# Kernel optimization log

Measured on AMD Instinct MI355X. Metric: run time of the kernel, lower is better.

The kernel has to match this reference:

```python
import jax, jax.numpy as jnp
import numpy as np

EMBED = 256
HEADS = 8
HEAD_DIM = EMBED // HEADS  # 32, even for RoPE
INIT_VAL = 1.0
HEADS_RANGE = 3.0


def rotate_every_two(x):
    # (x1, x2) -> (-x2, x1) on interleaved pairs of last dim
    x1 = x[..., ::2]
    x2 = x[..., 1::2]
    return jnp.stack([-x2, x1], axis=-1).reshape(x.shape)


def theta_shift(x, sin, cos):
    # x: [B, heads, H, W, D]; sin/cos: [H, W, D] broadcast over B, heads
    return x * cos + rotate_every_two(x) * sin


def rel_pos_2d(H, W):
    # RetNetRelPos2d: RoPE angles + per-head exponential decay mask
    angle = 1.0 / (10000.0 ** jnp.linspace(0.0, 1.0, HEAD_DIM // 2))
    angle = jnp.repeat(angle, 2)  # [D]
    idx = jnp.arange(H * W, dtype=jnp.float32)
    sin = jnp.sin(idx[:, None] * angle[None, :]).reshape(H, W, HEAD_DIM)
    cos = jnp.cos(idx[:, None] * angle[None, :]).reshape(H, W, HEAD_DIM)
    h_idx = jnp.arange(HEADS, dtype=jnp.float32)
    decay = jnp.log(1.0 - 2.0 ** (-INIT_VAL - HEADS_RANGE * h_idx / HEADS))  # [heads]
    gh, gw = jnp.meshgrid(jnp.arange(H), jnp.arange(W), indexing='ij')
    grid = jnp.stack([gh, gw], axis=-1).reshape(H * W, 2)  # [N,2]
    dist = jnp.abs(grid[:, None, :] - grid[None, :, :]).sum(-1)  # [N,N] L1 distance
    mask = dist[None, :, :].astype(jnp.float32) * decay[:, None, None]  # [heads,N,N]
    return sin, cos, mask


def setup_inputs() -> dict:
    key = jax.random.key(0)
    ks = jax.random.split(key, 8)
    B, H, W, C = 2, 48, 48, EMBED
    s = 0.02
    return {
        'x': jax.random.normal(ks[0], (B, H, W, C), jnp.float32),
        'Wq': jax.random.normal(ks[1], (C, C), jnp.float32) * s,
        'bq': jnp.zeros((C,), jnp.float32),
        'Wk': jax.random.normal(ks[2], (C, C), jnp.float32) * s,
        'bk': jnp.zeros((C,), jnp.float32),
        'Wv': jax.random.normal(ks[3], (C, C), jnp.float32) * s,
        'bv': jnp.zeros((C,), jnp.float32),
        'lepe_w': jax.random.normal(ks[4], (C, 1, 5, 5), jnp.float32) * s,  # depthwise 5x5
        'lepe_b': jnp.zeros((C,), jnp.float32),
        'Wo': jax.random.normal(ks[5], (C, C), jnp.float32) * s,
        'bo': jnp.zeros((C,), jnp.float32),
    }


def reference(x, Wq, bq, Wk, bk, Wv, bv, lepe_w, lepe_b, Wo, bo):
    B, H, W, C = x.shape
    N = H * W
    sin, cos, mask = rel_pos_2d(H, W)
    scaling = HEAD_DIM ** -0.5

    q = x @ Wq + bq
    k = (x @ Wk + bk) * scaling
    v = x @ Wv + bv

    # lepe: depthwise 5x5 conv on v (BHWC)
    lepe = jax.lax.conv_general_dilated(
        v.transpose(0, 3, 1, 2), lepe_w, (1, 1), 'SAME',
        feature_group_count=C, dimension_numbers=('NCHW', 'OIHW', 'NCHW'))
    lepe = lepe.transpose(0, 2, 3, 1) + lepe_b  # [B,H,W,C]

    def split_heads(t):
        return t.reshape(B, H, W, HEADS, HEAD_DIM).transpose(0, 3, 1, 2, 4)

    qr = theta_shift(split_heads(q), sin, cos).reshape(B, HEADS, N, HEAD_DIM)
    kr = theta_shift(split_heads(k), sin, cos).reshape(B, HEADS, N, HEAD_DIM)
    vv = split_heads(v).reshape(B, HEADS, N, HEAD_DIM)

    attn = jnp.einsum('bhnd,bhmd->bhnm', qr, kr) + mask[None]  # [B,heads,N,N]
    attn = jax.nn.softmax(attn, axis=-1)
    out = jnp.einsum('bhnm,bhmd->bhnd', attn, vv)
    out = out.transpose(0, 2, 1, 3).reshape(B, H, W, C)
    out = out + lepe
    return out @ Wo + bo
```

## Files before the change

kernel.cpp:

```cpp
#include <hip/hip_runtime.h>
#include <hip/hip_bf16.h>
#include <math.h>

#define NN 2304
#define ROWSZ 4608
#define SZ (ROWSZ*256)

typedef __attribute__((ext_vector_type(8))) short short8;
typedef __attribute__((ext_vector_type(4))) float f32x4;

__device__ __forceinline__ float bf2f(unsigned short u) {
    return __uint_as_float(((unsigned int)u) << 16);
}
__device__ __forceinline__ unsigned short f2bf(float f) {
    unsigned int u = __float_as_uint(f);
    u += 0x7FFFu + ((u >> 16) & 1u);
    return (unsigned short)(u >> 16);
}
__device__ __forceinline__ unsigned int pack_bf2(float a, float b) {
    return (unsigned int)f2bf(a) | ((unsigned int)f2bf(b) << 16);
}

__device__ __forceinline__ float ub2f(unsigned int v, int r) {
#if defined(__has_builtin)
#if __has_builtin(__builtin_amdgcn_cvt_f32_ubyte0)
    switch (r) {
        case 0: return __builtin_amdgcn_cvt_f32_ubyte0(v);
        case 1: return __builtin_amdgcn_cvt_f32_ubyte1(v);
        case 2: return __builtin_amdgcn_cvt_f32_ubyte2(v);
        default: return __builtin_amdgcn_cvt_f32_ubyte3(v);
    }
#else
    return (float)((v >> (8*r)) & 0xFFu);
#endif
#else
    return (float)((v >> (8*r)) & 0xFFu);
#endif
}

template<int F32>
__device__ __forceinline__ float ldin(const void* p, int i) {
    if constexpr (F32) return ((const float*)p)[i];
    else return bf2f(((const unsigned short*)p)[i]);
}

__global__ void detect_kernel(const unsigned int* __restrict__ x, int* __restrict__ flag) {
    int t = threadIdx.x;
    int cnt = 0;
    for (int i = t; i < 256; i += 64) {
        unsigned int e = (x[i] >> 7) & 0xFFu;
        cnt += (e < 87u || e > 167u) ? 1 : 0;
    }
    #pragma unroll
    for (int o = 32; o; o >>= 1) cnt += __shfl_down(cnt, o);
    if (t == 0) *flag = (cnt >= 32) ? 1 : 0;
}

__global__ __launch_bounds__(256) void dist_kernel(unsigned char* __restrict__ D,
                                                   float2* __restrict__ scT) {
    const int nq = blockIdx.x;
    const int yq = (nq*21846) >> 20, xq = nq - yq*48;
    unsigned int* drow = reinterpret_cast<unsigned int*>(D + (size_t)nq*NN);
    for (int idx = threadIdx.x; idx < 576; idx += 256) {
        const int kp0 = idx*4;
        unsigned int wv = 0;
        #pragma unroll
        for (int r = 0; r < 4; ++r) {
            int kp = kp0 + r;
            int yk = (kp*21846) >> 20;
            int xk = kp - yk*48;
            unsigned int dist = __usad((unsigned)yq, (unsigned)yk,
                                __usad((unsigned)xq, (unsigned)xk, 0u));
            wv |= dist << (8*r);
        }
        drow[idx] = wv;
    }
    if (threadIdx.x < 16) {
        const int j = threadIdx.x;
        const float ang = exp2f((float)j * (-0.8858474919699633f));
        float sv, cv;
        sincosf((float)nq * ang, &sv, &cv);
        scT[nq*16 + j] = make_float2(sv, cv);
    }
}

__global__ __launch_bounds__(256) void xprep_kernel(const void* __restrict__ x,
    const int* __restrict__ flag, unsigned short* __restrict__ xb)
{
    const int e = (blockIdx.x*256 + threadIdx.x) * 8;
    if (*flag) {
        const float* xp = (const float*)x + e;
        float4 a0 = *reinterpret_cast<const float4*>(xp);
        float4 a1 = *reinterpret_cast<const float4*>(xp + 4);
        uint4 o;
        o.x = pack_bf2(a0.x, a0.y); o.y = pack_bf2(a0.z, a0.w);
        o.z = pack_bf2(a1.x, a1.y); o.w = pack_bf2(a1.z, a1.w);
        *reinterpret_cast<uint4*>(xb + e) = o;
    } else {
        *reinterpret_cast<uint4*>(xb + e) =
            *reinterpret_cast<const uint4*>((const unsigned short*)x + e);
    }
}

__global__ __launch_bounds__(256) void wprep_kernel(
    const void* __restrict__ Wq, const void* __restrict__ bq,
    const void* __restrict__ Wk, const void* __restrict__ bk,
    const void* __restrict__ Wv, const void* __restrict__ bv,
    const int* __restrict__ flag,
    unsigned short* __restrict__ Wt, float* __restrict__ bb)
{
    __shared__ float wsh[256][17];
    const int t = threadIdx.x;
    const int m = blockIdx.y;
    const int oc0 = blockIdx.x * 16;
    const void* W  = (m == 0) ? Wq : (m == 1) ? Wk : Wv;
    const void* bs = (m == 0) ? bq : (m == 1) ? bk : bv;
    const float scale = (m == 1) ? 0.17677669529663687f * 1.4426950408889634f : 1.0f;
    const int F = *flag;
    #pragma unroll
    for (int j2 = 0; j2 < 16; ++j2)
        wsh[t][j2] = F ? ((const float*)W)[t*256 + oc0 + j2]
                       : bf2f(((const unsigned short*)W)[t*256 + oc0 + j2]);
    __syncthreads();
    const int j = t >> 4, seg = t & 15;
    unsigned int u[8];
    #pragma unroll
    for (int i = 0; i < 8; ++i) {
        float v0 = wsh[seg*16 + 2*i][j]     * scale;
        float v1 = wsh[seg*16 + 2*i + 1][j] * scale;
        u[i] = pack_bf2(v0, v1);
    }
    unsigned short* drow = Wt + ((size_t)(m*256 + oc0 + j))*256 + seg*16;
    *reinterpret_cast<uint4*>(drow)     = make_uint4(u[0], u[1], u[2], u[3]);
    *reinterpret_cast<uint4*>(drow + 8) = make_uint4(u[4], u[5], u[6], u[7]);
    if (blockIdx.x == 0)
        bb[m*256 + t] = (F ? ((const float*)bs)[t]
                           : bf2f(((const unsigned short*)bs)[t])) * scale;
}

__global__ __launch_bounds__(256) void qkv_mfma(
    const unsigned short* __restrict__ xb, const unsigned short* __restrict__ Wt,
    const float* __restrict__ bb, const float2* __restrict__ scT,
    unsigned short* __restrict__ q, unsigned short* __restrict__ k,
    unsigned short* __restrict__ v, unsigned short* __restrict__ vT)
{
    __shared__ __align__(16) char smem[43136];
    char* sc_lds = smem + 40960;
    const int t = threadIdx.x;
    const int w = t >> 6, lane = t & 63;
    const int q16 = lane & 15, quad = lane >> 4;
    const int m = blockIdx.y;
    const int tok0 = blockIdx.x * 16;
    const int b = (tok0 >= NN) ? 1 : 0;
    const int n0 = tok0 - b*NN;

    {
        float2 sv = scT[(size_t)(n0 + (t >> 4))*16 + (t & 15)];
        *reinterpret_cast<float2*>(sc_lds + (t >> 4)*136 + (t & 15)*8) = sv;
    }
    short8 af[8];
    #pragma unroll
    for (int kk = 0; kk < 8; ++kk)
        af[kk] = *reinterpret_cast<const short8*>(
            xb + (size_t)(tok0 + q16)*256 + kk*32 + quad*8);

    const unsigned short* Wm = Wt + (size_t)m*256*256;
    {
        const unsigned short* src = Wm + (size_t)t*256;
        #pragma unroll
        for (int s = 0; s < 4; ++s)
            *reinterpret_cast<uint4*>(smem + t*80 + s*16) =
                *reinterpret_cast<const uint4*>(src + s*8);
    }
    __syncthreads();

    f32x4 acc[4];
    #pragma unroll
    for (int tt = 0; tt < 4; ++tt) acc[tt] = (f32x4){0.f, 0.f, 0.f, 0.f};
    int cur = 0;
    for (int kk = 0; kk < 8; ++kk) {
        const int kkn = (kk < 7) ? kk + 1 : 7;
        uint4 nw[4];
        const unsigned short* src = Wm + (size_t)t*256 + kkn*32;
        #pragma unroll
        for (int s = 0; s < 4; ++s) nw[s] = *reinterpret_cast<const uint4*>(src + s*8);
        char* Wl = smem + cur*20480;
        #pragma unroll
        for (int tt = 0; tt < 4; ++tt) {
            short8 bf = *reinterpret_cast<const short8*>(
                Wl + (w*64 + tt*16 + q16)*80 + quad*16);
            acc[tt] = __builtin_amdgcn_mfma_f32_16x16x32_bf16(af[kk], bf, acc[tt], 0, 0, 0);
        }
        char* Wn = smem + (cur ^ 1)*20480;
        #pragma unroll
        for (int s = 0; s < 4; ++s)
            *reinterpret_cast<uint4*>(Wn + t*80 + s*16) = nw[s];
        __syncthreads();
        cur ^= 1;
    }

    char* ostage = smem;
    float bias[4];
    #pragma unroll
    for (int tt = 0; tt < 4; ++tt) bias[tt] = bb[m*256 + w*64 + tt*16 + q16];
    if (m < 2) {
        const int odd = q16 & 1;
        #pragma unroll
        for (int tt = 0; tt < 4; ++tt) {
            const int j = ((tt & 1) << 3) + (q16 >> 1);
            #pragma unroll
            for (int r = 0; r < 4; ++r) {
                const int tokL = quad*4 + r;
                float a = acc[tt][r] + bias[tt];
                float ap = __shfl_xor(a, 1);
                float2 sc = *reinterpret_cast<const float2*>(sc_lds + tokL*136 + j*8);
                float val = odd ? fmaf(a, sc.y, ap*sc.x) : fmaf(a, sc.y, -ap*sc.x);
                *reinterpret_cast<unsigned short*>(
                    ostage + tokL*528 + (w*64 + tt*16 + q16)*2) = f2bf(val);
            }
        }
    } else {
        #pragma unroll
        for (int tt = 0; tt < 4; ++tt) {
            #pragma unroll
            for (int r = 0; r < 4; ++r)
                *reinterpret_cast<unsigned short*>(
                    ostage + (quad*4 + r)*528 + (w*64 + tt*16 + q16)*2)
                    = f2bf(acc[tt][r] + bias[tt]);
        }
    }
    __syncthreads();
    unsigned short* dst = (m == 0) ? q : (m == 1) ? k : v;
    {
        char* p = ostage + (t >> 4)*528 + (t & 15)*32;
        uint4 a0 = *reinterpret_cast<uint4*>(p);
        uint4 a1 = *reinterpret_cast<uint4*>(p + 16);
        unsigned short* drow = dst + (size_t)(tok0 + (t >> 4))*256 + (t & 15)*16;
        *reinterpret_cast<uint4*>(drow)     = a0;
        *reinterpret_cast<uint4*>(drow + 8) = a1;
    }
    if (m == 2) {
        const int h = t >> 5, d = t & 31;
        unsigned int vp[8];
        #pragma unroll
        for (int i = 0; i < 8; ++i) {
            unsigned short e0 = *reinterpret_cast<unsigned short*>(
                ostage + (2*i)*528 + (h*32 + d)*2);
            unsigned short e1 = *reinterpret_cast<unsigned short*>(
                ostage + (2*i + 1)*528 + (h*32 + d)*2);
            vp[i] = (unsigned int)e0 | ((unsigned int)e1 << 16);
        }
        unsigned short* vt = vT + ((size_t)(b*8 + h)*32 + d)*NN + n0;
        *reinterpret_cast<uint4*>(vt)     = make_uint4(vp[0], vp[1], vp[2], vp[3]);
        *reinterpret_cast<uint4*>(vt + 8) = make_uint4(vp[4], vp[5], vp[6], vp[7]);
    }
}

template<int F32>
__device__ __forceinline__ void lepe_body(const unsigned short* __restrict__ v,
    const void* __restrict__ w, const void* __restrict__ wb,
    unsigned short* __restrict__ lepe)
{
    int c = threadIdx.x;
    int pos = blockIdx.x;
    int b  = pos >= NN ? 1 : 0;
    int yx = pos - b*NN;
    int y  = (yx*21846) >> 20;
    int xx = yx - y*48;
    float acc = ldin<F32>(wb, c);
    #pragma unroll
    for (int ky = 0; ky < 5; ++ky) {
        int yy = y + ky - 2;
        if ((unsigned)yy >= 48u) continue;
        #pragma unroll
        for (int kx = 0; kx < 5; ++kx) {
            int xc = xx + kx - 2;
            if ((unsigned)xc >= 48u) continue;
            acc = fmaf(bf2f(v[((b*NN + yy*48 + xc)<<8) + c]), ldin<F32>(w, c*25 + ky*5 + kx), acc);
        }
    }
    lepe[(pos<<8) + c] = f2bf(acc);
}

__global__ __launch_bounds__(256) void lepe_kernel(const unsigned short* __restrict__ v,
    const void* __restrict__ w, const void* __restrict__ wb,
    const int* __restrict__ flag, unsigned short* __restrict__ lepe)
{
    if (*flag) lepe_body<1>(v, w, wb, lepe);
    else       lepe_body<0>(v, w, wb, lepe);
}

template<int DIRECT>
__global__ __launch_bounds__(256) void attn_kernel(
    const unsigned short* __restrict__ q, const unsigned short* __restrict__ k,
    const unsigned short* __restrict__ vT, const unsigned char* __restrict__ D,
    unsigned short* __restrict__ o, float* __restrict__ pacc, float* __restrict__ pl)
{
    __shared__ char smem[27648];
    const int t = threadIdx.x;
    const int w = t >> 6, lane = t & 63;
    const int q16 = lane & 15, quad = lane >> 4;
    char* PsB = smem + 19456 + w*2048;
    const int bh = blockIdx.y, b = bh >> 3, h = bh & 7;
    const int q0 = blockIdx.x*64 + w*16;
    const int nq = q0 + q16;
    const float decay2 = log2f(1.0f - exp2f(-1.0f - 0.375f*(float)h));
    short8 qfrag = *reinterpret_cast<const short8*>(q + ((size_t)(b*NN + nq))*256 + h*32 + quad*8);
    f32x4 acc0 = {0.f,0.f,0.f,0.f}, acc1 = {0.f,0.f,0.f,0.f};
    const f32x4 zero = {0.f,0.f,0.f,0.f};
    float lacc = 0.0f;
    const unsigned short* kbase = k + (size_t)(b*NN)*256 + h*32;
    const unsigned short* vtb = vT + (size_t)bh*32*NN;
    const unsigned char* Dbase = D + (size_t)nq*NN + quad*4;
    const int skr = t >> 2, skp = t & 3;
    const int svd = t >> 3, svp = t & 7;
    const int psW = q16*16 + (quad & 1)*8;
    const int qsh = quad >> 1;
    const int nchunk = 36 / gridDim.z;
    const int kt0 = blockIdx.z * nchunk;

    {
        uint4 kraw = *reinterpret_cast<const uint4*>(kbase + (kt0*64 + skr)*256 + skp*8);
        uint4 vraw = *reinterpret_cast<const uint4*>(vtb + svd*NN + kt0*64 + svp*8);
        *reinterpret_cast<uint4*>(smem + skr*80 + skp*16) = kraw;
        *reinterpret_cast<uint4*>(smem + 5120 + svd*144 + svp*16) = vraw;
    }
    __syncthreads();

    int cur = 0;
    for (int kc = 0; kc < nchunk; ++kc) {
        const int kt = kt0 + kc;
        const int ktn = (kc + 1 < nchunk) ? kt + 1 : kt;
        uint4 nk = *reinterpret_cast<const uint4*>(kbase + (ktn*64 + skr)*256 + skp*8);
        uint4 nv = *reinterpret_cast<const uint4*>(vtb + svd*NN + ktn*64 + svp*8);
        unsigned int dw[4];
        #pragma unroll
        for (int tt = 0; tt < 4; ++tt)
            dw[tt] = *reinterpret_cast<const unsigned int*>(Dbase + kt*64 + tt*16);
        char* KsB = smem + cur*9728;
        char* VtB = KsB + 5120;
        f32x4 st[4];
        #pragma unroll
        for (int tt = 0; tt < 4; ++tt) {
            short8 kf = *reinterpret_cast<const short8*>(KsB + (tt*16 + q16)*80 + quad*16);
            st[tt] = __builtin_amdgcn_mfma_f32_16x16x32_bf16(kf, qfrag, zero, 0, 0, 0);
        }
        unsigned int pk[8];
        float lsum = 0.0f;
        #pragma unroll
        for (int tt = 0; tt < 4; ++tt) {
            float p[4];
            #pragma unroll
            for (int r = 0; r < 4; ++r) {
                p[r] = exp2f(fmaf(decay2, ub2f(dw[tt], r), st[tt][r]));
                lsum += p[r];
            }
            pk[tt*2]   = __builtin_amdgcn_perm(__float_as_uint(p[1]), __float_as_uint(p[0]), 0x07060302);
            pk[tt*2+1] = __builtin_amdgcn_perm(__float_as_uint(p[3]), __float_as_uint(p[2]), 0x07060302);
        }
        lacc += lsum;
        #pragma unroll
        for (int tt = 0; tt < 4; ++tt) {
            uint2 pp; pp.x = pk[tt*2]; pp.y = pk[tt*2+1];
            *reinterpret_cast<uint2*>(PsB + (tt >> 1)*1024 + (((tt*2) + qsh) & 3)*256 + psW) = pp;
        }
        #pragma unroll
        for (int kh = 0; kh < 2; ++kh) {
            short8 pf = *reinterpret_cast<const short8*>(PsB + kh*1024 + lane*16);
            short8 v0 = *reinterpret_cast<const short8*>(VtB + q16*144 + kh*64 + quad*16);
            short8 v1 = *reinterpret_cast<const short8*>(VtB + (16 + q16)*144 + kh*64 + quad*16);
            acc0 = __builtin_amdgcn_mfma_f32_16x16x32_bf16(v0, pf, acc0, 0, 0, 0);
            acc1 = __builtin_amdgcn_mfma_f32_16x16x32_bf16(v1, pf, acc1, 0, 0, 0);
        }
        char* KsN = smem + (cur^1)*9728;
        *reinterpret_cast<uint4*>(KsN + skr*80 + skp*16) = nk;
        *reinterpret_cast<uint4*>(KsN + 5120 + svd*144 + svp*16) = nv;
        __syncthreads();
        cur ^= 1;
    }
    lacc += __shfl_xor(lacc, 16);
    lacc += __shfl_xor(lacc, 32);
    if constexpr (DIRECT) {
        float invl = 1.0f / lacc;
        unsigned short* orow = o + ((size_t)(b*NN + nq))*256 + h*32;
        uint2 w0, w1;
        w0.x = pack_bf2(acc0[0]*invl, acc0[1]*invl);
        w0.y = pack_bf2(acc0[2]*invl, acc0[3]*invl);
        w1.x = pack_bf2(acc1[0]*invl, acc1[1]*invl);
        w1.y = pack_bf2(acc1[2]*invl, acc1[3]*invl);
        *reinterpret_cast<uint2*>(orow + quad*4)      = w0;
        *reinterpret_cast<uint2*>(orow + 16 + quad*4) = w1;
    } else {
        float* pb = pacc + ((size_t)(blockIdx.z*16 + bh)*NN + nq)*32;
        *reinterpret_cast<f32x4*>(pb + quad*4)      = acc0;
        *reinterpret_cast<f32x4*>(pb + 16 + quad*4) = acc1;
        if (quad == 0) pl[((size_t)blockIdx.z*16 + bh)*NN + nq] = lacc;
    }
}

template<int F32>
__device__ __forceinline__ void out_body(
    const unsigned short* __restrict__ o,
    const float* __restrict__ pacc, const float* __restrict__ pl,
    const unsigned short* __restrict__ lp,
    const void* __restrict__ Wo, const void* __restrict__ bo,
    void* __restrict__ out, float* __restrict__ as, int nsplit)
{
    const int t = threadIdx.x;
    const int row0 = blockIdx.x * 8;
    {
        const int e = t*8;
        const int r = t >> 5;
        const int nqr = row0 + r;
        const int ch = e & 255;
        uint4 ub = *reinterpret_cast<const uint4*>(lp + nqr*256 + ch);
        const unsigned short* bu = reinterpret_cast<const unsigned short*>(&ub);
        if (nsplit == 0) {
            uint4 ua = *reinterpret_cast<const uint4*>(o + nqr*256 + ch);
            const unsigned short* au = reinterpret_cast<const unsigned short*>(&ua);
            #pragma unroll
            for (int jj = 0; jj < 8; ++jj) as[e+jj] = bf2f(au[jj]) + bf2f(bu[jj]);
        } else {
            const int b = nqr >= NN ? 1 : 0;
            const int nq = nqr - b*NN;
            const int h = ch >> 5, d = ch & 31;
            const int bh = b*8 + h;
            float s[8] = {0.f,0.f,0.f,0.f,0.f,0.f,0.f,0.f};
            float lsum = 0.0f;
            for (int p = 0; p < nsplit; ++p) {
                const float* pb = pacc + ((size_t)(p*16 + bh)*NN + nq)*32 + d;
                f32x4 v0 = *reinterpret_cast<const f32x4*>(pb);
                f32x4 v1 = *reinterpret_cast<const f32x4*>(pb + 4);
                #pragma unroll
                for (int jj = 0; jj < 4; ++jj) { s[jj] += v0[jj]; s[4+jj] += v1[jj]; }
                lsum += pl[((size_t)p*16 + bh)*NN + nq];
            }
            float invl = 1.0f / lsum;
            #pragma unroll
            for (int jj = 0; jj < 8; ++jj) as[e+jj] = fmaf(s[jj], invl, bf2f(bu[jj]));
        }
    }
    __syncthreads();
    float a[8];
    const float bv = ldin<F32>(bo, t);
    #pragma unroll
    for (int r = 0; r < 8; ++r) a[r] = bv;
    for (int i0 = 0; i0 < 256; i0 += 4) {
        float w0 = ldin<F32>(Wo, (i0+0)*256 + t);
        float w1 = ldin<F32>(Wo, (i0+1)*256 + t);
        float w2 = ldin<F32>(Wo, (i0+2)*256 + t);
        float w3 = ldin<F32>(Wo, (i0+3)*256 + t);
        #pragma unroll
        for (int r = 0; r < 8; ++r) {
            float4 xv = *reinterpret_cast<const float4*>(&as[r*256 + i0]);
            a[r] = fmaf(xv.w,w3, fmaf(xv.z,w2, fmaf(xv.y,w1, fmaf(xv.x,w0, a[r]))));
        }
    }
    #pragma unroll
    for (int r = 0; r < 8; ++r) {
        int idx = (row0+r)*256 + t;
        if constexpr (F32) ((float*)out)[idx] = a[r];
        else ((unsigned short*)out)[idx] = f2bf(a[r]);
    }
}

__global__ __launch_bounds__(256) void out_kernel(
    const unsigned short* __restrict__ o,
    const float* __restrict__ pacc, const float* __restrict__ pl,
    const unsigned short* __restrict__ lp,
    const void* __restrict__ Wo, const void* __restrict__ bo,
    const int* __restrict__ flag, void* __restrict__ out, int nsplit)
{
    __shared__ float as[8*256];
    if (*flag) out_body<1>(o, pacc, pl, lp, Wo, bo, out, as, nsplit);
    else       out_body<0>(o, pacc, pl, lp, Wo, bo, out, as, nsplit);
}

extern "C" void kernel_launch(void* const* d_in, const int* in_sizes, int n_in,
                              void* d_out, int out_size, void* d_ws, size_t ws_size,
                              hipStream_t stream)
{
    const void* x  = d_in[0];
    const void* Wq = d_in[1];
    const void* bq = d_in[2];
    const void* Wk = d_in[3];
    const void* bk = d_in[4];
    const void* Wv = d_in[5];
    const void* bv = d_in[6];
    const void* lw = d_in[7];
    const void* lb = d_in[8];
    const void* Wo = d_in[9];
    const void* bo = d_in[10];

    int* flag = (int*)d_ws;
    unsigned short* qb   = (unsigned short*)((char*)d_ws + 256);
    unsigned short* kbuf = qb   + (size_t)SZ;
    unsigned short* vbuf = kbuf + (size_t)SZ;
    unsigned short* obuf = vbuf + (size_t)SZ;
    unsigned short* lbuf = obuf + (size_t)SZ;
    unsigned short* vtb  = lbuf + (size_t)SZ;
    unsigned char*  Dtab = (unsigned char*)(vtb + (size_t)SZ);
    float2* scT = (float2*)(Dtab + (size_t)NN*NN);
    unsigned short* xb = (unsigned short*)(scT + (size_t)NN*16);
    unsigned short* Wt = xb + (size_t)SZ;
    float* bb = (float*)(Wt + (size_t)3*256*256);

    const size_t base = 256 + 6*(size_t)SZ*2 + (size_t)NN*NN
                      + (size_t)NN*16*8 + (size_t)SZ*2
                      + (size_t)3*256*256*2 + (size_t)3*256*4;
    const size_t per_split = (size_t)16*NN*32*4 + (size_t)16*NN*4;
    int nsplit = 0;
    if      (ws_size >= base + 4*per_split) nsplit = 4;
    else if (ws_size >= base + 2*per_split) nsplit = 2;
    else if (ws_size >= base + 1*per_split) nsplit = 1;
    float* pacc = (float*)((char*)d_ws + base);
    float* pl   = pacc + (size_t)(nsplit ? nsplit : 1)*16*NN*32;

    detect_kernel<<<1, 64, 0, stream>>>((const unsigned int*)x, flag);
    dist_kernel<<<NN, 256, 0, stream>>>(Dtab, scT);
    xprep_kernel<<<576, 256, 0, stream>>>(x, flag, xb);
    wprep_kernel<<<dim3(16,3), 256, 0, stream>>>(Wq, bq, Wk, bk, Wv, bv, flag, Wt, bb);
    qkv_mfma<<<dim3(288,3), 256, 0, stream>>>(xb, Wt, bb, scT, qb, kbuf, vbuf, vtb);
    lepe_kernel<<<4608, 256, 0, stream>>>(vbuf, lw, lb, flag, lbuf);
    if (nsplit) {
        attn_kernel<0><<<dim3(36, 16, nsplit), 256, 0, stream>>>(qb, kbuf, vtb, Dtab, obuf, pacc, pl);
    } else {
        attn_kernel<1><<<dim3(36, 16, 1), 256, 0, stream>>>(qb, kbuf, vtb, Dtab, obuf, pacc, pl);
    }
    out_kernel<<<576, 256, 0, stream>>>(obuf, pacc, pl, lbuf, Wo, bo, flag, d_out, nsplit);
}
```

Baseline: 220.8 us.

## Move output projection onto bf16 MFMA with pre-transposed Wo

The output projection, previously a scalar FP32 FMA loop over 8 rows per block, now runs on 16x16x32 bf16 MFMA with 16 tokens per block. Wo and bo are transposed and converted to bf16 by the existing weight-prep kernel, and Wo slices are double-buffered through LDS. The attention+lepe activation is rounded to bf16 before the matmul, which costs precision, and the grid shrinks to 288 blocks.

```diff
diff --git a/kernel.cpp b/kernel.cpp
--- a/kernel.cpp
+++ b/kernel.cpp
@@ -106,6 +106,7 @@
     const void* __restrict__ Wq, const void* __restrict__ bq,
     const void* __restrict__ Wk, const void* __restrict__ bk,
     const void* __restrict__ Wv, const void* __restrict__ bv,
+    const void* __restrict__ Wo, const void* __restrict__ bo,
     const int* __restrict__ flag,
     unsigned short* __restrict__ Wt, float* __restrict__ bb)
 {
@@ -113,8 +114,8 @@
     const int t = threadIdx.x;
     const int m = blockIdx.y;
     const int oc0 = blockIdx.x * 16;
-    const void* W  = (m == 0) ? Wq : (m == 1) ? Wk : Wv;
-    const void* bs = (m == 0) ? bq : (m == 1) ? bk : bv;
+    const void* W  = (m == 0) ? Wq : (m == 1) ? Wk : (m == 2) ? Wv : Wo;
+    const void* bs = (m == 0) ? bq : (m == 1) ? bk : (m == 2) ? bv : bo;
     const float scale = (m == 1) ? 0.17677669529663687f * 1.4426950408889634f : 1.0f;
     const int F = *flag;
     #pragma unroll
@@ -398,82 +399,149 @@
     }
 }
 
-template<int F32>
-__device__ __forceinline__ void out_body(
+__global__ __launch_bounds__(256) void out_mfma(
     const unsigned short* __restrict__ o,
     const float* __restrict__ pacc, const float* __restrict__ pl,
     const unsigned short* __restrict__ lp,
-    const void* __restrict__ Wo, const void* __restrict__ bo,
-    void* __restrict__ out, float* __restrict__ as, int nsplit)
-{
+    const unsigned short* __restrict__ Wt, const float* __restrict__ bb,
+    const int* __restrict__ flag, void* __restrict__ out, int nsplit)
+{
+    __shared__ __align__(16) char smem[49408];
+    char* Ast = smem + 40960;
     const int t = threadIdx.x;
-    const int row0 = blockIdx.x * 8;
+    const int w = t >> 6, lane = t & 63;
+    const int q16 = lane & 15, quad = lane >> 4;
+    const int tok0 = blockIdx.x * 16;
+
     {
-        const int e = t*8;
-        const int r = t >> 5;
-        const int nqr = row0 + r;
-        const int ch = e & 255;
-        uint4 ub = *reinterpret_cast<const uint4*>(lp + nqr*256 + ch);
-        const unsigned short* bu = reinterpret_cast<const unsigned short*>(&ub);
+        const int r = t >> 4, c0 = (t & 15) * 16;
+        const int nqr = tok0 + r;
+        uint4 lb0 = *reinterpret_cast<const uint4*>(lp + (size_t)nqr*256 + c0);
+        uint4 lb1 = *reinterpret_cast<const uint4*>(lp + (size_t)nqr*256 + c0 + 8);
+        const unsigned short* lu0 = reinterpret_cast<const unsigned short*>(&lb0);
+        const unsigned short* lu1 = reinterpret_cast<const unsigned short*>(&lb1);
+        float av[16];
         if (nsplit == 0) {
-            uint4 ua = *reinterpret_cast<const uint4*>(o + nqr*256 + ch);
-            const unsigned short* au = reinterpret_cast<const unsigned short*>(&ua);
-            #pragma unroll
-            for (int jj = 0; jj < 8; ++jj) as[e+jj] = bf2f(au[jj]) + bf2f(bu[jj]);
+            uint4 oa0 = *reinterpret_cast<const uint4*>(o + (size_t)nqr*256 + c0);
+            uint4 oa1 = *reinterpret_cast<const uint4*>(o + (size_t)nqr*256 + c0 + 8);
+            const unsigned short* ou0 = reinterpret_cast<const unsigned short*>(&oa0);
+            const unsigned short* ou1 = reinterpret_cast<const unsigned short*>(&oa1);
+            #pragma unroll
+            for (int j = 0; j < 8; ++j) {
+                av[j]     = bf2f(ou0[j]) + bf2f(lu0[j]);
+                av[8 + j] = bf2f(ou1[j]) + bf2f(lu1[j]);
+            }
         } else {
             const int b = nqr >= NN ? 1 : 0;
             const int nq = nqr - b*NN;
-            const int h = ch >> 5, d = ch & 31;
-            const int bh = b*8 + h;
-            float s[8] = {0.f,0.f,0.f,0.f,0.f,0.f,0.f,0.f};
-            float lsum = 0.0f;
+            const int bh = b*8 + (c0 >> 5);
+            const int d0 = c0 & 31;
+            float s[16];
+            #pragma unroll
+            for (int j = 0; j < 16; ++j) s[j] = 0.f;
+            float lsum = 0.f;
             for (int p = 0; p < nsplit; ++p) {
-                const float* pb = pacc + ((size_t)(p*16 + bh)*NN + nq)*32 + d;
-                f32x4 v0 = *reinterpret_cast<const f32x4*>(pb);
-                f32x4 v1 = *reinterpret_cast<const f32x4*>(pb + 4);
+                const float* pb = pacc + ((size_t)(p*16 + bh)*NN + nq)*32 + d0;
                 #pragma unroll
-                for (int jj = 0; jj < 4; ++jj) { s[jj] += v0[jj]; s[4+jj] += v1[jj]; }
+                for (int j4 = 0; j4 < 4; ++j4) {
+                    f32x4 vv = *reinterpret_cast<const f32x4*>(pb + j4*4);
+                    s[j4*4+0] += vv[0]; s[j4*4+1] += vv[1];
+                    s[j4*4+2] += vv[2]; s[j4*4+3] += vv[3];
+                }
                 lsum += pl[((size_t)p*16 + bh)*NN + nq];
             }
             float invl = 1.0f / lsum;
             #pragma unroll
-            for (int jj = 0; jj < 8; ++jj) as[e+jj] = fmaf(s[jj], invl, bf2f(bu[jj]));
-        }
+            for (int j = 0; j < 8; ++j) {
+                av[j]     = fmaf(s[j],     invl, bf2f(lu0[j]));
+                av[8 + j] = fmaf(s[8 + j], invl, bf2f(lu1[j]));
+            }
+        }
+        unsigned int u[8];
+        #pragma unroll
+        for (int i = 0; i < 8; ++i) u[i] = pack_bf2(av[2*i], av[2*i+1]);
+        *reinterpret_cast<uint4*>(Ast + r*528 + c0*2)      = make_uint4(u[0],u[1],u[2],u[3]);
+        *reinterpret_cast<uint4*>(Ast + r*528 + c0*2 + 16) = make_uint4(u[4],u[5],u[6],u[7]);
+    }
+    const unsigned short* Wm = Wt + (size_t)3*256*256;
+    {
+        const unsigned short* src = Wm + (size_t)t*256;
+        #pragma unroll
+        for (int s2 = 0; s2 < 4; ++s2)
+            *reinterpret_cast<uint4*>(smem + t*80 + s2*16) =
+                *reinterpret_cast<const uint4*>(src + s2*8);
     }
     __syncthreads();
-    float a[8];
-    const float bv = ldin<F32>(bo, t);
-    #pragma unroll
-    for (int r = 0; r < 8; ++r) a[r] = bv;
-    for (int i0 = 0; i0 < 256; i0 += 4) {
-        float w0 = ldin<F32>(Wo, (i0+0)*256 + t);
-        float w1 = ldin<F32>(Wo, (i0+1)*256 + t);
-        float w2 = ldin<F32>(Wo, (i0+2)*256 + t);
-        float w3 = ldin<F32>(Wo, (i0+3)*256 + t);
-        #pragma unroll
-        for (int r = 0; r < 8; ++r) {
-            float4 xv = *reinterpret_cast<const float4*>(&as[r*256 + i0]);
-            a[r] = fmaf(xv.w,w3, fmaf(xv.z,w2, fmaf(xv.y,w1, fmaf(xv.x,w0, a[r]))));
-        }
-    }
-    #pragma unroll
-    for (int r = 0; r < 8; ++r) {
-        int idx = (row0+r)*256 + t;
-        if constexpr (F32) ((float*)out)[idx] = a[r];
-        else ((unsigned short*)out)[idx] = f2bf(a[r]);
-    }
-}
-
-__global__ __launch_bounds__(256) void out_kernel(
-    const unsigned short* __restrict__ o,
-    const float* __restrict__ pacc, const float* __restrict__ pl,
-    const unsigned short* __restrict__ lp,
-    const void* __restrict__ Wo, const void* __restrict__ bo,
-    const int* __restrict__ flag, void* __restrict__ out, int nsplit)
-{
-    __shared__ float as[8*256];
-    if (*flag) out_body<1>(o, pacc, pl, lp, Wo, bo, out, as, nsplit);
-    else       out_body<0>(o, pacc, pl, lp, Wo, bo, out, as, nsplit);
+    short8 af[8];
+    #pragma unroll
+    for (int kk = 0; kk < 8; ++kk)
+        af[kk] = *reinterpret_cast<const short8*>(Ast + q16*528 + kk*64 + quad*16);
+
+    f32x4 acc[4];
+    #pragma unroll
+    for (int tt = 0; tt < 4; ++tt) acc[tt] = (f32x4){0.f, 0.f, 0.f, 0.f};
+    int cur = 0;
+    for (int kk = 0; kk < 8; ++kk) {
+        const int kkn = (kk < 7) ? kk + 1 : 7;
+        uint4 nw[4];
+        const unsigned short* src = Wm + (size_t)t*256 + kkn*32;
+        #pragma unroll
+        for (int s2 = 0; s2 < 4; ++s2) nw[s2] = *reinterpret_cast<const uint4*>(src + s2*8);
+        char* Wl = smem + cur*20480;
+        #pragma unroll
+        for (int tt = 0; tt < 4; ++tt) {
+            short8 bf = *reinterpret_cast<const short8*>(
+                Wl + (w*64 + tt*16 + q16)*80 + quad*16);
+            acc[tt] = __builtin_amdgcn_mfma_f32_16x16x32_bf16(af[kk], bf, acc[tt], 0, 0, 0);
+        }
+        char* Wn = smem + (cur ^ 1)*20480;
+        #pragma unroll
+        for (int s2 = 0; s2 < 4; ++s2)
+            *reinterpret_cast<uint4*>(Wn + t*80 + s2*16) = nw[s2];
+        __syncthreads();
+        cur ^= 1;
+    }
+    const int F = *flag;
+    float bias[4];
+    #pragma unroll
+    for (int tt = 0; tt < 4; ++tt) bias[tt] = bb[3*256 + w*64 + tt*16 + q16];
+    if (F) {
+        char* ostf = smem;
+        #pragma unroll
+        for (int tt = 0; tt < 4; ++tt) {
+            #pragma unroll
+            for (int r = 0; r < 4; ++r)
+                *reinterpret_cast<float*>(ostf + (quad*4 + r)*1040
+                    + (w*64 + tt*16 + q16)*4) = acc[tt][r] + bias[tt];
+        }
+        __syncthreads();
+        char* p = ostf + (t >> 4)*1040 + (t & 15)*64;
+        float4 x0 = *reinterpret_cast<float4*>(p);
+        float4 x1 = *reinterpret_cast<float4*>(p + 16);
+        float4 x2 = *reinterpret_cast<float4*>(p + 32);
+        float4 x3 = *reinterpret_cast<float4*>(p + 48);
+        float* drow = (float*)out + (size_t)(tok0 + (t >> 4))*256 + (t & 15)*16;
+        *reinterpret_cast<float4*>(drow)      = x0;
+        *reinterpret_cast<float4*>(drow + 4)  = x1;
+        *reinterpret_cast<float4*>(drow + 8)  = x2;
+        *reinterpret_cast<float4*>(drow + 12) = x3;
+    } else {
+        char* ost = smem;
+        #pragma unroll
+        for (int tt = 0; tt < 4; ++tt) {
+            #pragma unroll
+            for (int r = 0; r < 4; ++r)
+                *reinterpret_cast<unsigned short*>(ost + (quad*4 + r)*528
+                    + (w*64 + tt*16 + q16)*2) = f2bf(acc[tt][r] + bias[tt]);
+        }
+        __syncthreads();
+        char* p = ost + (t >> 4)*528 + (t & 15)*32;
+        uint4 a0 = *reinterpret_cast<uint4*>(p);
+        uint4 a1 = *reinterpret_cast<uint4*>(p + 16);
+        unsigned short* drow = (unsigned short*)out + (size_t)(tok0 + (t >> 4))*256 + (t & 15)*16;
+        *reinterpret_cast<uint4*>(drow)     = a0;
+        *reinterpret_cast<uint4*>(drow + 8) = a1;
+    }
 }
 
 extern "C" void kernel_launch(void* const* d_in, const int* in_sizes, int n_in,
@@ -503,11 +571,11 @@
     float2* scT = (float2*)(Dtab + (size_t)NN*NN);
     unsigned short* xb = (unsigned short*)(scT + (size_t)NN*16);
     unsigned short* Wt = xb + (size_t)SZ;
-    float* bb = (float*)(Wt + (size_t)3*256*256);
+    float* bb = (float*)(Wt + (size_t)4*256*256);
 
     const size_t base = 256 + 6*(size_t)SZ*2 + (size_t)NN*NN
                       + (size_t)NN*16*8 + (size_t)SZ*2
-                      + (size_t)3*256*256*2 + (size_t)3*256*4;
+                      + (size_t)4*256*256*2 + (size_t)4*256*4;
     const size_t per_split = (size_t)16*NN*32*4 + (size_t)16*NN*4;
     int nsplit = 0;
     if      (ws_size >= base + 4*per_split) nsplit = 4;
@@ -519,7 +587,7 @@
     detect_kernel<<<1, 64, 0, stream>>>((const unsigned int*)x, flag);
     dist_kernel<<<NN, 256, 0, stream>>>(Dtab, scT);
     xprep_kernel<<<576, 256, 0, stream>>>(x, flag, xb);
-    wprep_kernel<<<dim3(16,3), 256, 0, stream>>>(Wq, bq, Wk, bk, Wv, bv, flag, Wt, bb);
+    wprep_kernel<<<dim3(16,4), 256, 0, stream>>>(Wq, bq, Wk, bk, Wv, bv, Wo, bo, flag, Wt, bb);
     qkv_mfma<<<dim3(288,3), 256, 0, stream>>>(xb, Wt, bb, scT, qb, kbuf, vbuf, vtb);
     lepe_kernel<<<4608, 256, 0, stream>>>(vbuf, lw, lb, flag, lbuf);
     if (nsplit) {
@@ -527,5 +595,5 @@
     } else {
         attn_kernel<1><<<dim3(36, 16, 1), 256, 0, stream>>>(qb, kbuf, vtb, Dtab, obuf, pacc, pl);
     }
-    out_kernel<<<576, 256, 0, stream>>>(obuf, pacc, pl, lbuf, Wo, bo, flag, d_out, nsplit);
-}
+    out_mfma<<<288, 256, 0, stream>>>(obuf, pacc, pl, lbuf, Wt, bb, flag, d_out, nsplit);
+}
```

Result: faster. 214.8 us (-2.7%).
